# Optimization experiments

Measured on AMD Instinct MI355X. Metric: run time of the kernel, lower is better.

## Reference

```python
import jax, jax.numpy as jnp
import numpy as np

POS_MARGIN = 0.01
NEG_MARGIN = 0.2
REG_WEIGHT = 0.1
N, D = 8192, 256
NUM_CLASSES = 512


def setup_inputs() -> dict:
    key = jax.random.key(0)
    k1, k2 = jax.random.split(key)
    embeds = jax.random.normal(k1, (N, D), dtype=jnp.float32)
    labels = jax.random.randint(k2, (N,), 0, NUM_CLASSES, dtype=jnp.int64)
    return {"embeds": embeds, "labels": labels}


def reference(embeds, labels):
    n, d = embeds.shape
    # L2-normalize embeddings (normalize_embeds=True)
    e = embeds / jnp.linalg.norm(embeds, axis=1, keepdims=True)

    # var(e_i - e_j, ddof=1) over feature dim, computed without the [N,N,D] tensor:
    # var = (D/(D-1)) * ( mean(e_i^2) + mean(e_j^2) - 2*mean(e_i*e_j) - (m_i - m_j)^2 )
    m = e.mean(axis=1)                      # [N]
    s = (e * e).mean(axis=1)                # [N]
    g = (e @ e.T) / d                       # [N,N] = mean(e_i * e_j) over D
    corr = d / (d - 1.0)
    var_diff = corr * (s[:, None] + s[None, :] - 2.0 * g - (m[:, None] - m[None, :]) ** 2)
    row_var = corr * (s - m * m)            # torch.var(e, dim=1), unbiased
    distmat = var_diff / row_var[:, None]

    same = labels[:, None] == labels[None, :]
    eye = jnp.eye(n, dtype=bool)
    pos_mask = same & (~eye)                # all same-label pairs (anchor != positive)
    neg_mask = ~same                        # all diff-label pairs

    pos_l = jax.nn.relu(distmat - POS_MARGIN) * pos_mask
    neg_l = jax.nn.relu(NEG_MARGIN - distmat) * neg_mask

    # avg_nonzero_only=True: sum / (# strictly-positive entries + 1e-12)
    pos_loss = pos_l.sum() / ((pos_l > 0).sum().astype(jnp.float32) + 1e-12)
    neg_loss = neg_l.sum() / ((neg_l > 0).sum().astype(jnp.float32) + 1e-12)

    loss = pos_loss + neg_loss
    loss = loss + jnp.abs(e.sum(axis=1)).mean() * REG_WEIGHT
    return loss
```

## Files before the change

### kernel.cpp

```cpp
#include <hip/hip_runtime.h>

#define NROWS 8192
#define DDIM 256
#define BT 64
#define BK 64
#define GT (NROWS / BT)
#define NBT (GT * (GT + 1) / 2)

using bf16x8 = __attribute__((ext_vector_type(8))) __bf16;
using f32x4  = __attribute__((ext_vector_type(4))) float;

__device__ __forceinline__ void glds16(const unsigned short* g, unsigned short* l) {
    __builtin_amdgcn_global_load_lds(
        (const __attribute__((address_space(1))) unsigned int*)g,
        (__attribute__((address_space(3))) unsigned int*)l,
        16, 0, 0);
}

__device__ __forceinline__ unsigned short f2bf(float f) {
    unsigned int b = __float_as_uint(f);
    unsigned int r = b + 0x7fffu + ((b >> 16) & 1u);
    return (unsigned short)(r >> 16);
}

__global__ __launch_bounds__(256) void rowstats_kernel(
    const float* __restrict__ x, unsigned short* __restrict__ ebf,
    float* __restrict__ aP, float* __restrict__ bs,
    float* __restrict__ rabs)
{
    int wave = threadIdx.x >> 6;
    int lane = threadIdx.x & 63;
    int row  = blockIdx.x * 4 + wave;

    const float4 v = reinterpret_cast<const float4*>(x + (size_t)row * DDIM)[lane];
    float ss = v.x * v.x + v.y * v.y + v.z * v.z + v.w * v.w;
    float sm = v.x + v.y + v.z + v.w;
    #pragma unroll
    for (int off = 32; off >= 1; off >>= 1) {
        ss += __shfl_xor(ss, off);
        sm += __shfl_xor(sm, off);
    }
    float invn = 1.0f / sqrtf(ss);
    float m = sm * invn * (1.0f / DDIM);

    ushort4 o;
    o.x = f2bf(v.x * invn - m);
    o.y = f2bf(v.y * invn - m);
    o.z = f2bf(v.z * invn - m);
    o.w = f2bf(v.w * invn - m);
    reinterpret_cast<ushort4*>(ebf + (size_t)row * DDIM)[lane] = o;

    if (lane == 0) {
        float s  = ss * invn * invn * (1.0f / DDIM);
        float b  = s - m * m;
        float a  = 1.0f / b;
        aP[row]   = a * (1.0f / 128.0f);
        bs[row]   = -128.0f * b;
        rabs[row] = fabsf(sm * invn);
    }
}

__global__ __launch_bounds__(256) void snr_gemm_kernel(
    const unsigned short* __restrict__ ebf,
    const float* __restrict__ aP, const float* __restrict__ bs,
    const int* __restrict__ labels,
    float* __restrict__ partials)
{
    __shared__ __align__(16) unsigned short As[BT * BK];
    __shared__ __align__(16) unsigned short Bs[BT * BK];
    __shared__ float sAPi[BT], sBsi[BT];
    __shared__ float sAPj[BT], sBsj[BT];
    __shared__ int   sLi[BT], sLj[BT];
    __shared__ float redbuf[4][4];

    int tid  = threadIdx.x;
    int lane = tid & 63;
    int wave = tid >> 6;
    int wr = (wave >> 1) * 32;
    int wc = (wave & 1) * 32;

    int t = blockIdx.x;
    int bi = (int)((2.0f * GT + 1.0f
                    - sqrtf((2.0f * GT + 1.0f) * (2.0f * GT + 1.0f) - 8.0f * (float)t)) * 0.5f);
    while ((bi + 1) * GT - ((bi + 1) * bi) / 2 <= t) ++bi;
    while (bi * GT - (bi * (bi - 1)) / 2 > t) --bi;
    int bj = bi + (t - (bi * GT - (bi * (bi - 1)) / 2));
    int rowBase = bi * BT, colBase = bj * BT;
    bool diag = (bi == bj);

    if (tid < BT) {
        int gi = rowBase + tid;
        sAPi[tid] = aP[gi]; sBsi[tid] = bs[gi];
        sLi[tid] = labels[gi];
    } else if (tid < 2 * BT) {
        int tt = tid - BT;
        int gj = colBase + tt;
        sAPj[tt] = aP[gj]; sBsj[tt] = bs[gj];
        sLj[tt] = labels[gj];
    }

    const unsigned short* gA[2];
    const unsigned short* gB[2];
    unsigned short* lpA[2];
    unsigned short* lpB[2];
    #pragma unroll
    for (int p = 0; p < 2; ++p) {
        int q   = p * 256 + tid;
        int row = q >> 3;
        int kc  = (q & 7) ^ (row & 7);
        gA[p] = ebf + (size_t)(rowBase + row) * DDIM + kc * 8;
        gB[p] = ebf + (size_t)(colBase + row) * DDIM + kc * 8;
        lpA[p] = As + q * 8;
        lpB[p] = Bs + q * 8;
    }

    int mrow = lane & 15;
    int kch  = lane >> 4;
    int offA[2][2], offB[2][2];
    #pragma unroll
    for (int t4 = 0; t4 < 2; ++t4) {
        int rA = wr + t4 * 16 + mrow;
        int rB = wc + t4 * 16 + mrow;
        #pragma unroll
        for (int h = 0; h < 2; ++h) {
            offA[t4][h] = (rA * 8 + ((h * 4 + kch) ^ (rA & 7))) * 8;
            offB[t4][h] = (rB * 8 + ((h * 4 + kch) ^ (rB & 7))) * 8;
        }
    }

    f32x4 acc[2][2];
    #pragma unroll
    for (int a = 0; a < 2; ++a)
        #pragma unroll
        for (int b = 0; b < 2; ++b)
            acc[a][b] = (f32x4){0.f, 0.f, 0.f, 0.f};

    for (int it = 0; it < 4; ++it) {
        #pragma unroll
        for (int p = 0; p < 2; ++p) {
            glds16(gA[p], lpA[p]);
            glds16(gB[p], lpB[p]);
            gA[p] += BK;
            gB[p] += BK;
        }
        asm volatile("s_waitcnt vmcnt(0)" ::: "memory");
        __syncthreads();

        #pragma unroll
        for (int h = 0; h < 2; ++h) {
            bf16x8 aF[2], bF[2];
            #pragma unroll
            for (int t4 = 0; t4 < 2; ++t4) {
                aF[t4] = *reinterpret_cast<const bf16x8*>(As + offA[t4][h]);
                bF[t4] = *reinterpret_cast<const bf16x8*>(Bs + offB[t4][h]);
            }
            #pragma unroll
            for (int ti = 0; ti < 2; ++ti)
                #pragma unroll
                for (int tj = 0; tj < 2; ++tj)
                    acc[ti][tj] = __builtin_amdgcn_mfma_f32_16x16x32_bf16(aF[ti], bF[tj], acc[ti][tj], 0, 0, 0);
        }
        __syncthreads();
    }

    int subr = (lane >> 4) * 4;
    int cj   = lane & 15;

    float aPC[2], bsC[2];
    int LCj[2];
    #pragma unroll
    for (int tj = 0; tj < 2; ++tj) {
        int lj = wc + tj * 16 + cj;
        aPC[tj] = sAPj[lj]; bsC[tj] = sBsj[lj];
        LCj[tj] = sLj[lj];
    }

    float Sn = 0.f, Sp = 0.f;
    unsigned Cn = 0u, Cp = 0u;

    if (!diag) {
        #pragma unroll
        for (int ti = 0; ti < 2; ++ti) {
            #pragma unroll
            for (int r = 0; r < 4; ++r) {
                int li = wr + ti * 16 + subr + r;
                float aR = sAPi[li], bR = sBsi[li];
                int LR = sLi[li];
                #pragma unroll
                for (int tj = 0; tj < 2; ++tj) {
                    float raw = acc[ti][tj][r];
                    float v1 = fmaf(aR, raw + bsC[tj], -0.8f);
                    float v2 = fmaf(aPC[tj], raw + bR, -0.8f);
                    bool same = (LR == LCj[tj]);
                    unsigned long long ms = __ballot(same);
                    float nz = fmaxf(v1, 0.f) + fmaxf(v2, 0.f);
                    Sn += same ? 0.f : nz;
                    float pz = fmaxf(0.19f - v1, 0.f) + fmaxf(0.19f - v2, 0.f);
                    Sp += same ? pz : 0.f;
                    Cn += (unsigned)__popcll(__ballot(v1 > 0.f) & ~ms)
                        + (unsigned)__popcll(__ballot(v2 > 0.f) & ~ms);
                    Cp += (unsigned)__popcll(__ballot(v1 < 0.19f) & ms)
                        + (unsigned)__popcll(__ballot(v2 < 0.19f) & ms);
                }
            }
        }
    } else {
        #pragma unroll
        for (int ti = 0; ti < 2; ++ti) {
            #pragma unroll
            for (int r = 0; r < 4; ++r) {
                int li = wr + ti * 16 + subr + r;
                float aR = sAPi[li];
                int LR = sLi[li];
                #pragma unroll
                for (int tj = 0; tj < 2; ++tj) {
                    int lj = wc + tj * 16 + cj;
                    float raw = acc[ti][tj][r];
                    float v1 = fmaf(aR, raw + bsC[tj], -0.8f);
                    bool same = (LR == LCj[tj]);
                    bool pok  = same && (li != lj);
                    unsigned long long ms = __ballot(same);
                    unsigned long long mp = __ballot(pok);
                    Sn += same ? 0.f : fmaxf(v1, 0.f);
                    float pz = fmaxf(0.19f - v1, 0.f);
                    Sp += pok ? pz : 0.f;
                    Cn += (unsigned)__popcll(__ballot(v1 > 0.f) & ~ms);
                    Cp += (unsigned)__popcll(__ballot(v1 < 0.19f) & mp);
                }
            }
        }
    }

    #pragma unroll
    for (int off = 32; off >= 1; off >>= 1) {
        Sn += __shfl_down(Sn, off);
        Sp += __shfl_down(Sp, off);
    }
    if (lane == 0) {
        redbuf[wave][0] = Sn; redbuf[wave][1] = (float)Cn;
        redbuf[wave][2] = Sp; redbuf[wave][3] = (float)Cp;
    }
    __syncthreads();
    if (tid < 4) {
        partials[blockIdx.x * 4 + tid] =
            redbuf[0][tid] + redbuf[1][tid] + redbuf[2][tid] + redbuf[3][tid];
    }
}

__global__ __launch_bounds__(256) void finalize_kernel(
    const float* __restrict__ partials, const float* __restrict__ rabs,
    float* __restrict__ out)
{
    int tid = threadIdx.x;
    float s0 = 0, s1 = 0, s2 = 0, s3 = 0, rr = 0;
    for (int i = tid; i < NBT; i += 256) {
        float4 p = reinterpret_cast<const float4*>(partials)[i];
        s0 += p.x; s1 += p.y; s2 += p.z; s3 += p.w;
    }
    for (int i = tid; i < NROWS; i += 256) rr += rabs[i];

    #pragma unroll
    for (int off = 32; off >= 1; off >>= 1) {
        s0 += __shfl_down(s0, off);
        s1 += __shfl_down(s1, off);
        s2 += __shfl_down(s2, off);
        s3 += __shfl_down(s3, off);
        rr += __shfl_down(rr, off);
    }
    __shared__ float red[4][5];
    int wave = tid >> 6, lane = tid & 63;
    if (lane == 0) {
        red[wave][0] = s0; red[wave][1] = s1; red[wave][2] = s2;
        red[wave][3] = s3; red[wave][4] = rr;
    }
    __syncthreads();
    if (tid == 0) {
        float a0 = 0, a1 = 0, a2 = 0, a3 = 0, a4 = 0;
        #pragma unroll
        for (int w = 0; w < 4; ++w) {
            a0 += red[w][0]; a1 += red[w][1]; a2 += red[w][2];
            a3 += red[w][3]; a4 += red[w][4];
        }
        float neg = (a1 > 0.5f) ? a0 / (a1 + 1e-12f) : 0.0f;
        float pos = (a3 > 0.5f) ? a2 / (a3 + 1e-12f) : 0.0f;
        out[0] = pos + neg + a4 * (0.1f / (float)NROWS);
    }
}

extern "C" void kernel_launch(void* const* d_in, const int* in_sizes, int n_in,
                              void* d_out, int out_size, void* d_ws, size_t ws_size,
                              hipStream_t stream) {
    const float* embeds = (const float*)d_in[0];
    const int*   labels = (const int*)d_in[1];
    float* out = (float*)d_out;

    char* ws = (char*)d_ws;
    unsigned short* ebf = (unsigned short*)ws;
    float* aP   = (float*)(ws + (size_t)NROWS * DDIM * 2);
    float* bs   = aP + NROWS;
    float* rabs = bs + NROWS;
    float* partials = rabs + NROWS;

    rowstats_kernel<<<NROWS / 4, 256, 0, stream>>>(embeds, ebf, aP, bs, rabs);

    snr_gemm_kernel<<<NBT, 256, 0, stream>>>(ebf, aP, bs, labels, partials);

    finalize_kernel<<<1, 256, 0, stream>>>(partials, rabs, out);
}
```

Before: 114.1 us.

## Double-buffer LDS tiles to overlap global loads with MFMA compute

Splits the A/B shared-memory tiles into two buffers and issues the next K-slice's global-to-LDS loads before computing on the current slice. The single barrier per iteration replaces the previous load-wait-compute-sync sequence, so memory latency can hide behind MFMA work. In exchange, LDS use doubles, which may reduce occupancy. The K loop is short (4 iterations), which limits how much overlap is available.

```diff
diff --git a/kernel.cpp b/kernel.cpp
--- a/kernel.cpp
+++ b/kernel.cpp
@@ -66,8 +66,8 @@
     const int* __restrict__ labels,
     float* __restrict__ partials)
 {
-    __shared__ __align__(16) unsigned short As[BT * BK];
-    __shared__ __align__(16) unsigned short Bs[BT * BK];
+    __shared__ __align__(16) unsigned short As[2][BT * BK];
+    __shared__ __align__(16) unsigned short Bs[2][BT * BK];
     __shared__ float sAPi[BT], sBsi[BT];
     __shared__ float sAPj[BT], sBsj[BT];
     __shared__ int   sLi[BT], sLj[BT];
@@ -101,8 +101,7 @@
 
     const unsigned short* gA[2];
     const unsigned short* gB[2];
-    unsigned short* lpA[2];
-    unsigned short* lpB[2];
+    int qoff[2];
     #pragma unroll
     for (int p = 0; p < 2; ++p) {
         int q   = p * 256 + tid;
@@ -110,8 +109,7 @@
         int kc  = (q & 7) ^ (row & 7);
         gA[p] = ebf + (size_t)(rowBase + row) * DDIM + kc * 8;
         gB[p] = ebf + (size_t)(colBase + row) * DDIM + kc * 8;
-        lpA[p] = As + q * 8;
-        lpB[p] = Bs + q * 8;
+        qoff[p] = q * 8;
     }
 
     int mrow = lane & 15;
@@ -135,24 +133,35 @@
         for (int b = 0; b < 2; ++b)
             acc[a][b] = (f32x4){0.f, 0.f, 0.f, 0.f};
 
+    #pragma unroll
+    for (int p = 0; p < 2; ++p) {
+        glds16(gA[p], &As[0][qoff[p]]);
+        glds16(gB[p], &Bs[0][qoff[p]]);
+        gA[p] += BK;
+        gB[p] += BK;
+    }
+    asm volatile("s_waitcnt vmcnt(0)" ::: "memory");
+    __syncthreads();
+
+    #pragma unroll
     for (int it = 0; it < 4; ++it) {
-        #pragma unroll
-        for (int p = 0; p < 2; ++p) {
-            glds16(gA[p], lpA[p]);
-            glds16(gB[p], lpB[p]);
-            gA[p] += BK;
-            gB[p] += BK;
-        }
-        asm volatile("s_waitcnt vmcnt(0)" ::: "memory");
-        __syncthreads();
-
+        int cur = it & 1;
+        if (it < 3) {
+            #pragma unroll
+            for (int p = 0; p < 2; ++p) {
+                glds16(gA[p], &As[cur ^ 1][qoff[p]]);
+                glds16(gB[p], &Bs[cur ^ 1][qoff[p]]);
+                gA[p] += BK;
+                gB[p] += BK;
+            }
+        }
         #pragma unroll
         for (int h = 0; h < 2; ++h) {
             bf16x8 aF[2], bF[2];
             #pragma unroll
             for (int t4 = 0; t4 < 2; ++t4) {
-                aF[t4] = *reinterpret_cast<const bf16x8*>(As + offA[t4][h]);
-                bF[t4] = *reinterpret_cast<const bf16x8*>(Bs + offB[t4][h]);
+                aF[t4] = *reinterpret_cast<const bf16x8*>(&As[cur][0] + offA[t4][h]);
+                bF[t4] = *reinterpret_cast<const bf16x8*>(&Bs[cur][0] + offB[t4][h]);
             }
             #pragma unroll
             for (int ti = 0; ti < 2; ++ti)
@@ -160,7 +169,10 @@
                 for (int tj = 0; tj < 2; ++tj)
                     acc[ti][tj] = __builtin_amdgcn_mfma_f32_16x16x32_bf16(aF[ti], bF[tj], acc[ti][tj], 0, 0, 0);
         }
-        __syncthreads();
+        if (it < 3) {
+            asm volatile("s_waitcnt vmcnt(0)" ::: "memory");
+            __syncthreads();
+        }
     }
 
     int subr = (lane >> 4) * 4;
```

Result: slower. 120.9 us (+6.0%).
